# Kernel optimization log

Measured on AMD Instinct MI355X. Metric: run time of the kernel, lower is better.

Reference implementation:

```python
import jax, jax.numpy as jnp
import numpy as np

B = 65536
D_MODEL = 2048
N_EXPERTS = 64
TOP_K = 8
AUX_COEF = 0.01


def setup_inputs() -> dict:
    key = jax.random.key(0)
    kx, kw = jax.random.split(key)
    x = jax.random.normal(kx, (B, D_MODEL), dtype=jnp.float32)
    # nn.Linear(d_model, n_experts, bias=False); stored here as (d_model, n_experts)
    W = jax.random.normal(kw, (D_MODEL, N_EXPERTS), dtype=jnp.float32) / np.sqrt(D_MODEL).astype(np.float32)
    expert_bias = jnp.zeros((N_EXPERTS,), dtype=jnp.float32)
    return {"x": x, "W": W, "expert_bias": expert_bias}


def reference(x, W, expert_bias):
    # router logits: (B, n_experts)
    logits = x @ W
    # topk on bias-shifted logits (aux-loss-free balancing bias)
    biased = logits + expert_bias
    _, indices = jax.lax.top_k(biased, TOP_K)              # (B, top_k) int32
    # softmax over the UNbiased logits of the selected experts
    selected = jnp.take_along_axis(logits, indices, axis=-1)  # (B, top_k)
    gates_topk = jax.nn.softmax(selected, axis=-1)
    # scatter gate weights into sparse (B, n_experts) tensor
    rows = jnp.arange(logits.shape[0])[:, None]
    gates = jnp.zeros_like(logits).at[rows, indices].set(gates_topk)
    # aux load-balance loss (training mode): fraction routed * mean prob
    f_i = (gates > 0).astype(logits.dtype).mean(axis=0)       # (n_experts,)
    P_i = jax.nn.softmax(logits, axis=-1).mean(axis=0)        # (n_experts,)
    aux_loss = AUX_COEF * N_EXPERTS * jnp.sum(f_i * P_i)
    return gates, indices, aux_loss
```

## Files before the change

### kernel.cpp

```cpp
#include <hip/hip_runtime.h>
#include <cstdint>
#include <cstddef>

typedef __attribute__((ext_vector_type(8))) short short8;
typedef __attribute__((ext_vector_type(4))) float f32x4;

#define B_ROWS 65536
#define DMODEL 2048
#define NEXP 64
#define TOPK 8
#define THREADS 256
#define ROWS_PER_BLK 64
#define NBLK (B_ROWS / ROWS_PER_BLK)
#define NKS (DMODEL / 32)
#define SLAB 67
#define GOFF ((size_t)B_ROWS * NEXP)
#define AUX_OFF (GOFF + (size_t)B_ROWS * TOPK)
#define WS_FRAG_OFF 131072
#define WS2_OFF 229376
#define XW 2080
#define BBASE 8320
#define LDSF 14464

#define GLOAD16(g, l)                                                      \
  __builtin_amdgcn_global_load_lds(                                       \
      (const __attribute__((address_space(1))) void*)(g),                 \
      (__attribute__((address_space(3))) void*)(l), 16, 0, 0)

__device__ __forceinline__ unsigned short bf16_rne(float v, float* back) {
  unsigned u = __float_as_uint(v);
  unsigned r = (u + 0x7FFFu + ((u >> 16) & 1u)) >> 16;
  *back = __uint_as_float(r << 16);
  return (unsigned short)r;
}

__global__ __launch_bounds__(256) void router_prep(
    const float* __restrict__ W, unsigned short* __restrict__ frag)
{
  const int ks = blockIdx.x;
  const int nt = threadIdx.x >> 6;
  const int lane = threadIdx.x & 63;
  const int krow = ks * 32 + (lane >> 4) * 8;
  const int col = nt * 16 + (lane & 15);
  short8 hv, mv, lv;
#pragma unroll
  for (int j = 0; j < 8; ++j) {
    float v = W[(size_t)(krow + j) * NEXP + col];
    float fh, fm, fl;
    unsigned short h = bf16_rne(v, &fh);
    float r = v - fh;
    unsigned short m = bf16_rne(r, &fm);
    float r2 = r - fm;
    unsigned short l = bf16_rne(r2, &fl);
    hv[j] = (short)h; mv[j] = (short)m; lv[j] = (short)l;
  }
  size_t base = (size_t)(ks * 4 + nt) * 1536 + lane * 8;
  *(short8*)(frag + base)        = hv;
  *(short8*)(frag + base + 512)  = mv;
  *(short8*)(frag + base + 1024) = lv;
}

__device__ __forceinline__ void cvt3(float4 a, float4 b,
                                     short8* H, short8* M, short8* L) {
  float f[8] = {a.x, a.y, a.z, a.w, b.x, b.y, b.z, b.w};
#pragma unroll
  for (int j = 0; j < 8; ++j) {
    float fh, fm, fl;
    unsigned short h = bf16_rne(f[j], &fh);
    float r = f[j] - fh;
    unsigned short m = bf16_rne(r, &fm);
    float r2 = r - fm;
    unsigned short l = bf16_rne(r2, &fl);
    (*H)[j] = (short)h; (*M)[j] = (short)m; (*L)[j] = (short)l;
  }
}

#define MFMA __builtin_amdgcn_mfma_f32_16x16x32_bf16

__global__ __launch_bounds__(THREADS, 2) void router_main(
    const float* __restrict__ x, const float* __restrict__ bias,
    const unsigned short* __restrict__ frag, float* __restrict__ out,
    float* __restrict__ ws)
{
  __shared__ __align__(16) float lds[LDSF];

  const int tid = threadIdx.x;
  const int lane = tid & 63;
  const int w = tid >> 6;
  const size_t row0 = (size_t)blockIdx.x * ROWS_PER_BLK;

  f32x4 acc[4];
#pragma unroll
  for (int nt = 0; nt < 4; ++nt) acc[nt] = (f32x4){0.f, 0.f, 0.f, 0.f};

  const float* xg = x + (row0 + (size_t)w * 16 + (lane >> 5)) * DMODEL
                  + (lane & 31) * 4;
  const int xr_off = w * XW + ((lane & 15) >> 1) * 260 + ((lane & 15) & 1) * 128
                   + (lane >> 4) * 8;

#define STAGE_X(SC)                                                        \
  do {                                                                     \
    _Pragma("unroll") for (int i = 0; i < 8; ++i)                          \
      GLOAD16(xg + (size_t)i * 2 * DMODEL + (SC) * 128,                    \
              lds + w * XW + i * 260);                                     \
  } while (0)

#define STAGE_B(KS, BUF)                                                   \
  do {                                                                     \
    _Pragma("unroll") for (int j = 0; j < 3; ++j)                          \
      GLOAD16(frag + (size_t)(KS) * 6144 + (w * 3 + j) * 512 + lane * 8,   \
              lds + BBASE + (BUF) * 3072 + (w * 3 + j) * 256);             \
  } while (0)

  STAGE_X(0);
  STAGE_B(0, 0);

  for (int ks = 0; ks < NKS; ++ks) {
    __syncthreads();
    if ((ks & 3) == 0 && ks > 0) {
      STAGE_X(ks >> 2);
      if (ks + 1 < NKS) STAGE_B(ks + 1, (ks + 1) & 1);
      asm volatile("s_waitcnt vmcnt(3)" ::: "memory");
      __builtin_amdgcn_sched_barrier(0);
    } else {
      if (ks + 1 < NKS) STAGE_B(ks + 1, (ks + 1) & 1);
    }

    const float* bb = lds + BBASE + (ks & 1) * 3072;
    short8 B[12];
#pragma unroll
    for (int f = 0; f < 12; ++f)
      B[f] = *(const short8*)(bb + f * 256 + lane * 4);

    float4 c0 = *(const float4*)(lds + xr_off + (ks & 3) * 32);
    float4 c1 = *(const float4*)(lds + xr_off + (ks & 3) * 32 + 4);
    short8 Ah, Am, Al;
    cvt3(c0, c1, &Ah, &Am, &Al);
#pragma unroll
    for (int nt = 0; nt < 4; ++nt) {
      acc[nt] = MFMA(Ah, B[nt * 3 + 0], acc[nt], 0, 0, 0);
      acc[nt] = MFMA(Ah, B[nt * 3 + 1], acc[nt], 0, 0, 0);
      acc[nt] = MFMA(Am, B[nt * 3 + 0], acc[nt], 0, 0, 0);
      acc[nt] = MFMA(Am, B[nt * 3 + 1], acc[nt], 0, 0, 0);
      acc[nt] = MFMA(Ah, B[nt * 3 + 2], acc[nt], 0, 0, 0);
      acc[nt] = MFMA(Al, B[nt * 3 + 0], acc[nt], 0, 0, 0);
    }
  }

  __syncthreads();
  float* slab = lds;
#pragma unroll
  for (int nt = 0; nt < 4; ++nt)
#pragma unroll
    for (int reg = 0; reg < 4; ++reg) {
      int row = w * 16 + (lane >> 4) * 4 + reg;
      int col = nt * 16 + (lane & 15);
      slab[row * SLAB + col] = acc[nt][reg];
    }
  __syncthreads();

  if (w == 0) {
    float a[NEXP];
#pragma unroll
    for (int n = 0; n < NEXP; ++n) a[n] = slab[lane * SLAB + n];

    unsigned long long sel = 0ull;
    int idx[TOPK];
    float selu[TOPK];
#pragma unroll
    for (int k = 0; k < TOPK; ++k) {
      float best = -INFINITY, bestu = 0.f;
      int bi = 0;
#pragma unroll
      for (int n = 0; n < NEXP; ++n) {
        float vb = a[n] + bias[n];
        bool taken = (sel >> n) & 1ull;
        vb = taken ? -INFINITY : vb;
        if (vb > best) { best = vb; bestu = a[n]; bi = n; }
      }
      sel |= 1ull << bi;
      idx[k] = bi;
      selu[k] = bestu;
    }

    float mx = selu[0];
#pragma unroll
    for (int k = 1; k < TOPK; ++k) mx = fmaxf(mx, selu[k]);
    float g[TOPK]; float gs = 0.f;
#pragma unroll
    for (int k = 0; k < TOPK; ++k) { g[k] = __expf(selu[k] - mx); gs += g[k]; }
    float ginv = 1.f / gs;

    float* grow = out + (row0 + lane) * NEXP;
#pragma unroll
    for (int n4 = 0; n4 < 16; ++n4) {
      float gv[4];
#pragma unroll
      for (int j = 0; j < 4; ++j) {
        int n = n4 * 4 + j;
        float v = 0.f;
#pragma unroll
        for (int k = 0; k < TOPK; ++k) v = (idx[k] == n) ? g[k] * ginv : v;
        gv[j] = v;
      }
      *(float4*)(grow + n4 * 4) = make_float4(gv[0], gv[1], gv[2], gv[3]);
    }

    float* irow = out + GOFF + (row0 + lane) * TOPK;
    *(float4*)(irow + 0) = make_float4((float)idx[0], (float)idx[1], (float)idx[2], (float)idx[3]);
    *(float4*)(irow + 4) = make_float4((float)idx[4], (float)idx[5], (float)idx[6], (float)idx[7]);

    float m2 = -INFINITY;
#pragma unroll
    for (int n = 0; n < NEXP; ++n) m2 = fmaxf(m2, a[n]);
    float s2 = 0.f;
#pragma unroll
    for (int n = 0; n < NEXP; ++n) s2 += __expf(a[n] - m2);
    float pinv = 1.f / s2;

    float myP = 0.f, myF = 0.f;
#pragma unroll
    for (int n = 0; n < NEXP; ++n) {
      float v = __expf(a[n] - m2) * pinv;
      v += __shfl_xor(v, 1);
      v += __shfl_xor(v, 2);
      v += __shfl_xor(v, 4);
      v += __shfl_xor(v, 8);
      v += __shfl_xor(v, 16);
      v += __shfl_xor(v, 32);
      unsigned long long b = __ballot((sel >> n) & 1ull);
      if (lane == n) { myP = v; myF = (float)__popcll(b); }
    }
    ws[(size_t)blockIdx.x * (2 * NEXP) + lane] = myF;
    ws[(size_t)blockIdx.x * (2 * NEXP) + NEXP + lane] = myP;
  }
}

__global__ __launch_bounds__(256) void router_aux1(
    const float* __restrict__ ws, float* __restrict__ ws2)
{
  __shared__ float sf[4][NEXP];
  __shared__ float sp[4][NEXP];
  int t = threadIdx.x;
  int n = t & 63, part = t >> 6;
  int b0 = blockIdx.x * 64;
  float f = 0.f, p = 0.f;
#pragma unroll 4
  for (int b = b0 + part; b < b0 + 64; b += 4) {
    f += ws[(size_t)b * (2 * NEXP) + n];
    p += ws[(size_t)b * (2 * NEXP) + NEXP + n];
  }
  sf[part][n] = f;
  sp[part][n] = p;
  __syncthreads();
  if (t < NEXP) {
    ws2[blockIdx.x * 128 + t]      = sf[0][t] + sf[1][t] + sf[2][t] + sf[3][t];
    ws2[blockIdx.x * 128 + 64 + t] = sp[0][t] + sp[1][t] + sp[2][t] + sp[3][t];
  }
}

__global__ __launch_bounds__(64) void router_aux2(
    const float* __restrict__ ws2, float* __restrict__ out)
{
  int t = threadIdx.x;
  float F = 0.f, P = 0.f;
#pragma unroll
  for (int g = 0; g < 16; ++g) {
    F += ws2[g * 128 + t];
    P += ws2[g * 128 + 64 + t];
  }
  float v = F * P;
  v += __shfl_xor(v, 1);
  v += __shfl_xor(v, 2);
  v += __shfl_xor(v, 4);
  v += __shfl_xor(v, 8);
  v += __shfl_xor(v, 16);
  v += __shfl_xor(v, 32);
  if (t == 0)
    out[AUX_OFF] = 0.01f * 64.f * v / (4294967296.0f );
}

extern "C" void kernel_launch(void* const* d_in, const int* in_sizes, int n_in,
                              void* d_out, int out_size, void* d_ws, size_t ws_size,
                              hipStream_t stream) {
  const float* x = (const float*)d_in[0];
  const float* W = (const float*)d_in[1];
  const float* bias = (const float*)d_in[2];
  float* out = (float*)d_out;
  float* ws = (float*)d_ws;
  unsigned short* frag = (unsigned short*)(ws + WS_FRAG_OFF);
  float* ws2 = ws + WS2_OFF;
  router_prep<<<NKS, 256, 0, stream>>>(W, frag);
  router_main<<<NBLK, THREADS, 0, stream>>>(x, bias, frag, out, ws);
  router_aux1<<<16, 256, 0, stream>>>(ws, ws2);
  router_aux2<<<1, 64, 0, stream>>>(ws2, out);
}
```

Measured before the change: 232.8 us.

## Load router weight fragments from global directly and double-buffer x per wave

```diff
diff --git a/kernel.cpp b/kernel.cpp
--- a/kernel.cpp
+++ b/kernel.cpp
@@ -13,14 +13,13 @@
 #define ROWS_PER_BLK 64
 #define NBLK (B_ROWS / ROWS_PER_BLK)
 #define NKS (DMODEL / 32)
+#define NSC 16
+#define XW 2080
 #define SLAB 67
 #define GOFF ((size_t)B_ROWS * NEXP)
 #define AUX_OFF (GOFF + (size_t)B_ROWS * TOPK)
 #define WS_FRAG_OFF 131072
 #define WS2_OFF 229376
-#define XW 2080
-#define BBASE 8320
-#define LDSF 14464
 
 #define GLOAD16(g, l)                                                      \
   __builtin_amdgcn_global_load_lds(                                       \
@@ -82,7 +81,7 @@
     const unsigned short* __restrict__ frag, float* __restrict__ out,
     float* __restrict__ ws)
 {
-  __shared__ __align__(16) float lds[LDSF];
+  __shared__ __align__(16) float lds[4 * 2 * XW];
 
   const int tid = threadIdx.x;
   const int lane = tid & 63;
@@ -95,56 +94,65 @@
 
   const float* xg = x + (row0 + (size_t)w * 16 + (lane >> 5)) * DMODEL
                   + (lane & 31) * 4;
-  const int xr_off = w * XW + ((lane & 15) >> 1) * 260 + ((lane & 15) & 1) * 128
-                   + (lane >> 4) * 8;
-
-#define STAGE_X(SC)                                                        \
+  const int xrbase = w * (2 * XW) + ((lane & 15) >> 1) * 260
+                   + ((lane & 15) & 1) * 128 + (lane >> 4) * 8;
+
+#define STAGE_X(SC, BUF)                                                   \
   do {                                                                     \
     _Pragma("unroll") for (int i = 0; i < 8; ++i)                          \
       GLOAD16(xg + (size_t)i * 2 * DMODEL + (SC) * 128,                    \
-              lds + w * XW + i * 260);                                     \
-  } while (0)
-
-#define STAGE_B(KS, BUF)                                                   \
-  do {                                                                     \
-    _Pragma("unroll") for (int j = 0; j < 3; ++j)                          \
-      GLOAD16(frag + (size_t)(KS) * 6144 + (w * 3 + j) * 512 + lane * 8,   \
-              lds + BBASE + (BUF) * 3072 + (w * 3 + j) * 256);             \
-  } while (0)
-
-  STAGE_X(0);
-  STAGE_B(0, 0);
-
-  for (int ks = 0; ks < NKS; ++ks) {
-    __syncthreads();
-    if ((ks & 3) == 0 && ks > 0) {
-      STAGE_X(ks >> 2);
-      if (ks + 1 < NKS) STAGE_B(ks + 1, (ks + 1) & 1);
-      asm volatile("s_waitcnt vmcnt(3)" ::: "memory");
-      __builtin_amdgcn_sched_barrier(0);
-    } else {
-      if (ks + 1 < NKS) STAGE_B(ks + 1, (ks + 1) & 1);
-    }
-
-    const float* bb = lds + BBASE + (ks & 1) * 3072;
-    short8 B[12];
-#pragma unroll
-    for (int f = 0; f < 12; ++f)
-      B[f] = *(const short8*)(bb + f * 256 + lane * 4);
-
-    float4 c0 = *(const float4*)(lds + xr_off + (ks & 3) * 32);
-    float4 c1 = *(const float4*)(lds + xr_off + (ks & 3) * 32 + 4);
-    short8 Ah, Am, Al;
-    cvt3(c0, c1, &Ah, &Am, &Al);
-#pragma unroll
-    for (int nt = 0; nt < 4; ++nt) {
-      acc[nt] = MFMA(Ah, B[nt * 3 + 0], acc[nt], 0, 0, 0);
-      acc[nt] = MFMA(Ah, B[nt * 3 + 1], acc[nt], 0, 0, 0);
-      acc[nt] = MFMA(Am, B[nt * 3 + 0], acc[nt], 0, 0, 0);
-      acc[nt] = MFMA(Am, B[nt * 3 + 1], acc[nt], 0, 0, 0);
-      acc[nt] = MFMA(Ah, B[nt * 3 + 2], acc[nt], 0, 0, 0);
-      acc[nt] = MFMA(Al, B[nt * 3 + 0], acc[nt], 0, 0, 0);
-    }
+              lds + w * (2 * XW) + (BUF) * XW + i * 260);                  \
+  } while (0)
+
+#define LOAD_B(KS, NT, BH, BM, BL)                                         \
+  do {                                                                     \
+    const short8* fb_ = (const short8*)(frag + (size_t)((KS) * 4 + (NT)) * 1536); \
+    BH = fb_[lane]; BM = fb_[lane + 64]; BL = fb_[lane + 128];             \
+  } while (0)
+
+#define MFMA12(NT, BH, BM, BL)                                             \
+  do {                                                                     \
+    acc[NT] = MFMA(Ah, BH, acc[NT], 0, 0, 0);                              \
+    acc[NT] = MFMA(Ah, BM, acc[NT], 0, 0, 0);                              \
+    acc[NT] = MFMA(Am, BH, acc[NT], 0, 0, 0);                              \
+    acc[NT] = MFMA(Am, BM, acc[NT], 0, 0, 0);                              \
+    acc[NT] = MFMA(Ah, BL, acc[NT], 0, 0, 0);                              \
+    acc[NT] = MFMA(Al, BH, acc[NT], 0, 0, 0);                              \
+  } while (0)
+
+#define KS_BODY(S, KK, BUF)                                                \
+  do {                                                                     \
+    const int ks_ = (S) * 4 + (KK);                                        \
+    short8 BhA, BmA, BlA, BhB, BmB, BlB;                                   \
+    LOAD_B(ks_, 0, BhA, BmA, BlA);                                         \
+    float4 c0 = *(const float4*)(lds + xrbase + (BUF) * XW + (KK) * 32);   \
+    float4 c1 = *(const float4*)(lds + xrbase + (BUF) * XW + (KK) * 32 + 4);\
+    short8 Ah, Am, Al;                                                     \
+    cvt3(c0, c1, &Ah, &Am, &Al);                                           \
+    LOAD_B(ks_, 1, BhB, BmB, BlB);                                         \
+    MFMA12(0, BhA, BmA, BlA);                                              \
+    LOAD_B(ks_, 2, BhA, BmA, BlA);                                         \
+    MFMA12(1, BhB, BmB, BlB);                                              \
+    LOAD_B(ks_, 3, BhB, BmB, BlB);                                         \
+    MFMA12(2, BhA, BmA, BlA);                                              \
+    MFMA12(3, BhB, BmB, BlB);                                              \
+  } while (0)
+
+#define SC_BODY(S, CUR)                                                    \
+  do {                                                                     \
+    asm volatile("s_waitcnt vmcnt(0)" ::: "memory");                       \
+    __builtin_amdgcn_sched_barrier(0);                                     \
+    if ((S) + 1 < NSC) STAGE_X((S) + 1, (CUR) ^ 1);                        \
+    KS_BODY(S, 0, CUR);                                                    \
+    KS_BODY(S, 1, CUR);                                                    \
+    KS_BODY(S, 2, CUR);                                                    \
+    KS_BODY(S, 3, CUR);                                                    \
+  } while (0)
+
+  STAGE_X(0, 0);
+  for (int s2 = 0; s2 < NSC / 2; ++s2) {
+    SC_BODY(s2 * 2, 0);
+    SC_BODY(s2 * 2 + 1, 1);
   }
 
   __syncthreads();
```

Result: slower. 271.4 us (+16.6%).
